# Performance work log

Measured on AMD Instinct MI355X. Metric: run time of the kernel, lower is better.

Reference implementation:

```python
import jax, jax.numpy as jnp
import numpy as np

N_HEAD = 16
N_KV = 4
N_EMBD = 2048
HEAD_DIM = N_EMBD // N_HEAD  # 128
GROUP = N_HEAD // N_KV       # 4 queries per kv head


def setup_inputs() -> dict:
    key = jax.random.key(0)
    ks = jax.random.split(key, 5)
    B, S = 2, 2048
    scale = 0.02
    return {
        "x": jax.random.normal(ks[0], (B, S, N_EMBD), dtype=jnp.float32),
        "Wq": jax.random.normal(ks[1], (N_EMBD, N_EMBD), dtype=jnp.float32) * scale,
        "Wk": jax.random.normal(ks[2], (N_EMBD, N_EMBD // GROUP), dtype=jnp.float32) * scale,
        "Wv": jax.random.normal(ks[3], (N_EMBD, N_EMBD // GROUP), dtype=jnp.float32) * scale,
        "Wo": jax.random.normal(ks[4], (N_EMBD, N_EMBD), dtype=jnp.float32) * scale,
    }


def reference(x, Wq, Wk, Wv, Wo):
    B, S, _ = x.shape
    scale = HEAD_DIM ** -0.5
    # projections (bias=False)
    q = (x @ Wq).reshape(B, S, N_KV, GROUP, HEAD_DIM)   # grouped query heads
    k = (x @ Wk).reshape(B, S, N_KV, HEAD_DIM)
    v = (x @ Wv).reshape(B, S, N_KV, HEAD_DIM)
    # scores: repeat_interleave of K over GROUP == broadcast over g axis
    scores = jnp.einsum('bqkgd,bskd->bkgqs', q, k) * scale  # [B,n_kv,g,S,S]
    causal = jnp.triu(jnp.ones((S, S), dtype=bool), k=1)
    scores = jnp.where(causal, jnp.finfo(scores.dtype).min, scores)
    attn = jax.nn.softmax(scores, axis=-1)
    out = jnp.einsum('bkgqs,bskd->bqkgd', attn, v)  # [B,S,n_kv,g,hd]
    out = out.reshape(B, S, N_EMBD)
    return out @ Wo
```

## Files before the change

kernel.cpp:

```cpp
#include <hip/hip_runtime.h>

typedef unsigned short u16;
typedef unsigned int u32;
typedef __attribute__((ext_vector_type(8))) __bf16 bh8;
typedef __attribute__((ext_vector_type(4))) float fx4;

#define AS1 __attribute__((address_space(1)))
#define AS3 __attribute__((address_space(3)))

__device__ __forceinline__ void gll16(const void* g, void* l) {
  void* gg = const_cast<void*>(g);
  __builtin_amdgcn_global_load_lds((AS1 void*)gg, (AS3 void*)l, 16, 0, 0);
}

__device__ __forceinline__ u16 f2b(float f) {
  union { float f; u32 u; } v; v.f = f;
  u32 r = v.u + 0x7FFFu + ((v.u >> 16) & 1u);
  return (u16)(r >> 16);
}

__device__ __forceinline__ fx4 fzero() { fx4 z = {0.f, 0.f, 0.f, 0.f}; return z; }

#define MFMA16(a, b, c) __builtin_amdgcn_mfma_f32_16x16x32_bf16(a, b, c, 0, 0, 0)

__global__ void k_cast(const float* __restrict__ in, u16* __restrict__ out, int n4) {
  int i = blockIdx.x * blockDim.x + threadIdx.x;
  if (i >= n4) return;
  float4 v = reinterpret_cast<const float4*>(in)[i];
  ushort4 o;
  o.x = f2b(v.x); o.y = f2b(v.y); o.z = f2b(v.z); o.w = f2b(v.w);
  reinterpret_cast<ushort4*>(out)[i] = o;
}

__global__ void k_transpose_cast(const float* __restrict__ in, u16* __restrict__ out,
                                 int R, int C) {
  __shared__ float t[32][33];
  int tx = threadIdx.x, ty = threadIdx.y;
  int r0 = blockIdx.y * 32, c0 = blockIdx.x * 32;
#pragma unroll
  for (int j = 0; j < 4; j++)
    t[ty + 8 * j][tx] = in[(size_t)(r0 + ty + 8 * j) * C + c0 + tx];
  __syncthreads();
#pragma unroll
  for (int j = 0; j < 4; j++)
    out[(size_t)(c0 + ty + 8 * j) * R + r0 + tx] = f2b(t[tx][ty + 8 * j]);
}

__global__ void k_transpose_v(const u16* __restrict__ in, u16* __restrict__ out) {
  __shared__ u16 t[32][33];
  int tx = threadIdx.x, ty = threadIdx.y;
  int s0 = blockIdx.x * 32, d0 = blockIdx.y * 32;
  int z = blockIdx.z, b = z >> 2, kv = z & 3;
#pragma unroll
  for (int j = 0; j < 4; j++)
    t[ty + 8 * j][tx] = in[(size_t)(b * 2048 + s0 + ty + 8 * j) * 512 + kv * 128 + d0 + tx];
  __syncthreads();
#pragma unroll
  for (int j = 0; j < 4; j++)
    out[(size_t)(z * 128 + d0 + ty + 8 * j) * 2048 + s0 + tx] = t[tx][ty + 8 * j];
}

__device__ __forceinline__ void gemm_core(const u16* __restrict__ A, const u16* __restrict__ Bt,
                                          int bm, int bn, u16* As, u16* Bs, fx4 acc[4][4]) {
  const int tid = threadIdx.x;
  const int lane = tid & 63, w = tid >> 6;
  const int wr = w >> 1, wc = w & 1;
  const int i = lane & 15, g = lane >> 4;
  const int c0 = tid, c1 = tid + 256;
  const u16* ga0 = A + (size_t)(bm + (c0 >> 2)) * 2048 + (c0 & 3) * 8;
  const u16* ga1 = A + (size_t)(bm + (c1 >> 2)) * 2048 + (c1 & 3) * 8;
  const u16* gb0 = Bt + (size_t)(bn + (c0 >> 2)) * 2048 + (c0 & 3) * 8;
  const u16* gb1 = Bt + (size_t)(bn + (c1 >> 2)) * 2048 + (c1 & 3) * 8;
  u16* la0 = As + c0 * 8; u16* la1 = As + c1 * 8;
  u16* lb0 = Bs + c0 * 8; u16* lb1 = Bs + c1 * 8;
  const u16* ra = As + (wr * 64 + i) * 32 + g * 8;
  const u16* rb = Bs + (wc * 64 + i) * 32 + g * 8;
  for (int kt = 0; kt < 2048; kt += 32) {
    __syncthreads();
    gll16(ga0 + kt, la0);
    gll16(ga1 + kt, la1);
    gll16(gb0 + kt, lb0);
    gll16(gb1 + kt, lb1);
    __syncthreads();
    bh8 af[4], bfr[4];
#pragma unroll
    for (int m = 0; m < 4; m++) af[m] = *reinterpret_cast<const bh8*>(ra + m * 16 * 32);
#pragma unroll
    for (int n = 0; n < 4; n++) bfr[n] = *reinterpret_cast<const bh8*>(rb + n * 16 * 32);
#pragma unroll
    for (int m = 0; m < 4; m++)
#pragma unroll
      for (int n = 0; n < 4; n++)
        acc[m][n] = MFMA16(af[m], bfr[n], acc[m][n]);
  }
}

__global__ __launch_bounds__(256, 3) void k_proj(const u16* __restrict__ xb,
                                                 const u16* __restrict__ Wqt,
                                                 const u16* __restrict__ Wkt,
                                                 const u16* __restrict__ Wvt,
                                                 u16* __restrict__ Qb, u16* __restrict__ Kb,
                                                 u16* __restrict__ Vb) {
  __shared__ __align__(16) u16 As[128 * 32];
  __shared__ __align__(16) u16 Bs[128 * 32];
  int by = blockIdx.y;
  const u16* Bt; u16* Cp; int bn, ldc; float alpha;
  if (by < 16)      { Bt = Wqt; Cp = Qb; bn = by * 128;        ldc = 2048; alpha = 0.08838834764831845f; }
  else if (by < 20) { Bt = Wkt; Cp = Kb; bn = (by - 16) * 128; ldc = 512;  alpha = 1.0f; }
  else              { Bt = Wvt; Cp = Vb; bn = (by - 20) * 128; ldc = 512;  alpha = 1.0f; }
  int bm = blockIdx.x * 128;
  fx4 acc[4][4];
#pragma unroll
  for (int m = 0; m < 4; m++)
#pragma unroll
    for (int n = 0; n < 4; n++) acc[m][n] = fzero();
  gemm_core(xb, Bt, bm, bn, As, Bs, acc);
  const int lane = threadIdx.x & 63, w = threadIdx.x >> 6;
  const int wr = w >> 1, wc = w & 1, i = lane & 15, g = lane >> 4;
#pragma unroll
  for (int m = 0; m < 4; m++)
#pragma unroll
    for (int n = 0; n < 4; n++)
#pragma unroll
      for (int r = 0; r < 4; r++) {
        int row = bm + wr * 64 + m * 16 + 4 * g + r;
        int col = bn + wc * 64 + n * 16 + i;
        Cp[(size_t)row * ldc + col] = f2b(acc[m][n][r] * alpha);
      }
}

__global__ __launch_bounds__(256, 3) void k_gemm_out(const u16* __restrict__ Ob,
                                                     const u16* __restrict__ Wot,
                                                     float* __restrict__ C) {
  __shared__ __align__(16) u16 As[128 * 32];
  __shared__ __align__(16) u16 Bs[128 * 32];
  int bm = blockIdx.x * 128, bn = blockIdx.y * 128;
  fx4 acc[4][4];
#pragma unroll
  for (int m = 0; m < 4; m++)
#pragma unroll
    for (int n = 0; n < 4; n++) acc[m][n] = fzero();
  gemm_core(Ob, Wot, bm, bn, As, Bs, acc);
  const int lane = threadIdx.x & 63, w = threadIdx.x >> 6;
  const int wr = w >> 1, wc = w & 1, i = lane & 15, g = lane >> 4;
#pragma unroll
  for (int m = 0; m < 4; m++)
#pragma unroll
    for (int n = 0; n < 4; n++)
#pragma unroll
      for (int r = 0; r < 4; r++) {
        int row = bm + wr * 64 + m * 16 + 4 * g + r;
        int col = bn + wc * 64 + n * 16 + i;
        C[(size_t)row * 2048 + col] = acc[m][n][r];
      }
}

__global__ __launch_bounds__(512, 4) void k_attn(const u16* __restrict__ Qb,
                                                 const u16* __restrict__ Kb,
                                                 const u16* __restrict__ Vt,
                                                 u16* __restrict__ Ob) {
  __shared__ __align__(16) u16 Ks0[64 * 128], Ks1[64 * 128];
  __shared__ __align__(16) u16 Vs0[128 * 64], Vs1[128 * 64];
  __shared__ __align__(16) u16 Pl[8][16 * 64];
  const int tid = threadIdx.x, lane = tid & 63, w = tid >> 6;
  const int i = lane & 15, g = lane >> 4;
  const int j = blockIdx.x;
  const int head = blockIdx.y, b = blockIdx.z, kv = head >> 2;
  const bool isA = (w >= 4);
  const int qt = isA ? j : (31 - j);
  const int qmin = qt * 64 + (w & 3) * 16;
  const int nt = 32 - j;
  const int myNt = isA ? (j + 1) : nt;

  const u16* Kbb = Kb + (size_t)b * 2048 * 512 + kv * 128;
  const u16* Vbb = Vt + (size_t)(b * 4 + kv) * 128 * 2048;

  bh8 qf[4];
  {
    const u16* qp = Qb + (size_t)(b * 2048 + qmin + i) * 2048 + head * 128 + g * 8;
#pragma unroll
    for (int kb = 0; kb < 4; kb++) qf[kb] = *reinterpret_cast<const bh8*>(qp + kb * 32);
  }

  fx4 o[8];
#pragma unroll
  for (int dt = 0; dt < 8; dt++) o[dt] = fzero();
  float m[4] = {-1e30f, -1e30f, -1e30f, -1e30f};
  float lp[4] = {0.f, 0.f, 0.f, 0.f};

  auto STAGE = [&](u16* Kd, u16* Vd, int s0) {
#pragma unroll
    for (int cc = 0; cc < 2; cc++) {
      int c = tid + cc * 512;
      gll16(Kbb + (size_t)(s0 + (c >> 4)) * 512 + (((c & 15) ^ ((c >> 4) & 7)) * 8),
            Kd + c * 8);
      gll16(Vbb + (size_t)(c >> 3) * 2048 + s0 + (((c & 7) ^ ((c >> 3) & 7)) * 8),
            Vd + c * 8);
    }
  };

  auto TILE = [&](const u16* Kbuf, const u16* Vbuf, int s0) {
    fx4 sc[4];
    __builtin_amdgcn_s_setprio(1);
#pragma unroll
    for (int st = 0; st < 4; st++) {
      sc[st] = fzero();
#pragma unroll
      for (int kb = 0; kb < 4; kb++) {
        bh8 kf = *reinterpret_cast<const bh8*>(Kbuf + (st * 16 + i) * 128 +
                                               (((kb * 4 + g) ^ (i & 7)) * 8));
        sc[st] = MFMA16(qf[kb], kf, sc[st]);
      }
    }
    __builtin_amdgcn_s_setprio(0);
    if (s0 + 63 > qmin) {
#pragma unroll
      for (int st = 0; st < 4; st++)
#pragma unroll
        for (int r = 0; r < 4; r++) {
          int s = s0 + st * 16 + i;
          int q = qmin + 4 * g + r;
          if (s > q) sc[st][r] = -1e30f;
        }
    }
    float pmax[4];
#pragma unroll
    for (int r = 0; r < 4; r++) {
      float v = fmaxf(fmaxf(sc[0][r], sc[1][r]), fmaxf(sc[2][r], sc[3][r]));
      v = fmaxf(v, __shfl_xor(v, 1));
      v = fmaxf(v, __shfl_xor(v, 2));
      v = fmaxf(v, __shfl_xor(v, 4));
      v = fmaxf(v, __shfl_xor(v, 8));
      pmax[r] = v;
    }
    int need = 0;
#pragma unroll
    for (int r = 0; r < 4; r++) need |= (pmax[r] > m[r] + 8.0f) ? 1 : 0;
    if (__any(need)) {
#pragma unroll
      for (int r = 0; r < 4; r++) {
        float mn = fmaxf(m[r], pmax[r]);
        float corr = __expf(m[r] - mn);
        m[r] = mn;
        lp[r] *= corr;
#pragma unroll
        for (int dt = 0; dt < 8; dt++) o[dt][r] *= corr;
      }
    }
    float p[4][4];
#pragma unroll
    for (int r = 0; r < 4; r++) {
#pragma unroll
      for (int st = 0; st < 4; st++) p[st][r] = __expf(sc[st][r] - m[r]);
      lp[r] += (p[0][r] + p[1][r]) + (p[2][r] + p[3][r]);
    }

#pragma unroll
    for (int st = 0; st < 4; st++)
#pragma unroll
      for (int r = 0; r < 4; r++) {
        int row = 4 * g + r;
        int cg = st * 2 + (i >> 3);
        Pl[w][row * 64 + ((cg ^ (row & 7)) << 3) + (i & 7)] = f2b(p[st][r]);
      }
    bh8 pf0 = *reinterpret_cast<const bh8*>(&Pl[w][i * 64 + ((g ^ (i & 7)) << 3)]);
    bh8 pf1 = *reinterpret_cast<const bh8*>(&Pl[w][i * 64 + (((4 + g) ^ (i & 7)) << 3)]);
    __builtin_amdgcn_s_setprio(1);
#pragma unroll
    for (int dt = 0; dt < 8; dt++) {
      bh8 v0 = *reinterpret_cast<const bh8*>(Vbuf + (dt * 16 + i) * 64 +
                                             ((g ^ (i & 7)) * 8));
      bh8 v1 = *reinterpret_cast<const bh8*>(Vbuf + (dt * 16 + i) * 64 +
                                             (((4 + g) ^ (i & 7)) * 8));
      o[dt] = MFMA16(pf0, v0, o[dt]);
      o[dt] = MFMA16(pf1, v1, o[dt]);
    }
    __builtin_amdgcn_s_setprio(0);
  };

  STAGE(Ks0, Vs0, 0);
  __syncthreads();
  for (int t = 0; t < nt; t += 2) {
    if (t + 1 < nt) STAGE(Ks1, Vs1, (t + 1) * 64);
    if (t < myNt) TILE(Ks0, Vs0, t * 64);
    __syncthreads();
    if (t + 1 >= nt) break;
    if (t + 2 < nt) STAGE(Ks0, Vs0, (t + 2) * 64);
    if (t + 1 < myNt) TILE(Ks1, Vs1, (t + 1) * 64);
    __syncthreads();
  }

#pragma unroll
  for (int r = 0; r < 4; r++) {
    float s = lp[r];
    s += __shfl_xor(s, 1);
    s += __shfl_xor(s, 2);
    s += __shfl_xor(s, 4);
    s += __shfl_xor(s, 8);
    float inv = 1.0f / s;
#pragma unroll
    for (int dt = 0; dt < 8; dt++)
      Ob[(size_t)(b * 2048 + qmin + 4 * g + r) * 2048 + head * 128 + dt * 16 + i] =
          f2b(o[dt][r] * inv);
  }
}

extern "C" void kernel_launch(void* const* d_in, const int* in_sizes, int n_in,
                              void* d_out, int out_size, void* d_ws, size_t ws_size,
                              hipStream_t stream) {
  (void)in_sizes; (void)n_in; (void)out_size; (void)ws_size;
  const float* x  = (const float*)d_in[0];
  const float* Wq = (const float*)d_in[1];
  const float* Wk = (const float*)d_in[2];
  const float* Wv = (const float*)d_in[3];
  const float* Wo = (const float*)d_in[4];

  char* ws = (char*)d_ws;
  size_t off = 0;
  auto alloc = [&](size_t bytes) {
    void* p = ws + off;
    off += (bytes + 255) & ~(size_t)255;
    return p;
  };
  u16* xb  = (u16*)alloc(8388608ull * 2);
  u16* Wqt = (u16*)alloc(4194304ull * 2);
  u16* Wkt = (u16*)alloc(1048576ull * 2);
  u16* Wvt = (u16*)alloc(1048576ull * 2);
  u16* Wot = (u16*)alloc(4194304ull * 2);
  u16* Qb  = (u16*)alloc(8388608ull * 2);
  u16* Kb  = (u16*)alloc(2097152ull * 2);
  u16* Vb  = (u16*)alloc(2097152ull * 2);
  u16* Vt  = (u16*)alloc(2097152ull * 2);
  u16* Ob  = xb;

  k_cast<<<8192, 256, 0, stream>>>(x, xb, 2097152);
  k_transpose_cast<<<dim3(64, 64), dim3(32, 8), 0, stream>>>(Wq, Wqt, 2048, 2048);
  k_transpose_cast<<<dim3(16, 64), dim3(32, 8), 0, stream>>>(Wk, Wkt, 2048, 512);
  k_transpose_cast<<<dim3(16, 64), dim3(32, 8), 0, stream>>>(Wv, Wvt, 2048, 512);
  k_transpose_cast<<<dim3(64, 64), dim3(32, 8), 0, stream>>>(Wo, Wot, 2048, 2048);
  k_proj<<<dim3(32, 24), 256, 0, stream>>>(xb, Wqt, Wkt, Wvt, Qb, Kb, Vb);
  k_transpose_v<<<dim3(64, 4, 8), dim3(32, 8), 0, stream>>>(Vb, Vt);
  k_attn<<<dim3(16, 16, 2), 512, 0, stream>>>(Qb, Kb, Vt, Ob);
  k_gemm_out<<<dim3(32, 16), 256, 0, stream>>>(Ob, Wot, (float*)d_out);
}
```

Baseline: 330.0 us.

## Use 256x256 double-buffered swizzled GEMM tiles for projection and output GEMMs

Replaces the 128x128, BK=32, single-buffered GEMM core with a 256x256 tile computed by 512 threads. It uses BK=64, XOR-swizzled LDS, and double buffering, so the next tile's global-to-LDS loads are issued between MFMA groups, with s_setprio raised around the MFMAs. The Q/K/V projections now index one concatenated transposed weight through a single pointer, which relies on Wkt and Wvt sitting right after Wqt in memory. The aim is more data reuse per LDS load and hidden load latency. The cost is far fewer blocks: 192 for the projection and 128 for the output GEMM, which may leave many CUs idle.

```diff
diff --git a/kernel.cpp b/kernel.cpp
--- a/kernel.cpp
+++ b/kernel.cpp
@@ -60,98 +60,126 @@
     out[(size_t)(z * 128 + d0 + ty + 8 * j) * 2048 + s0 + tx] = t[tx][ty + 8 * j];
 }
 
-__device__ __forceinline__ void gemm_core(const u16* __restrict__ A, const u16* __restrict__ Bt,
-                                          int bm, int bn, u16* As, u16* Bs, fx4 acc[4][4]) {
+__device__ __forceinline__ void gemm256(const u16* __restrict__ A, const u16* __restrict__ Bt,
+                                        int bm, int bn, u16* Sm, fx4 (&acc)[8][4]) {
+  u16* As = Sm;
+  u16* Bs = Sm + 32768;
   const int tid = threadIdx.x;
-  const int lane = tid & 63, w = tid >> 6;
-  const int wr = w >> 1, wc = w & 1;
+  const int lane = tid & 63;
   const int i = lane & 15, g = lane >> 4;
-  const int c0 = tid, c1 = tid + 256;
-  const u16* ga0 = A + (size_t)(bm + (c0 >> 2)) * 2048 + (c0 & 3) * 8;
-  const u16* ga1 = A + (size_t)(bm + (c1 >> 2)) * 2048 + (c1 & 3) * 8;
-  const u16* gb0 = Bt + (size_t)(bn + (c0 >> 2)) * 2048 + (c0 & 3) * 8;
-  const u16* gb1 = Bt + (size_t)(bn + (c1 >> 2)) * 2048 + (c1 & 3) * 8;
-  u16* la0 = As + c0 * 8; u16* la1 = As + c1 * 8;
-  u16* lb0 = Bs + c0 * 8; u16* lb1 = Bs + c1 * 8;
-  const u16* ra = As + (wr * 64 + i) * 32 + g * 8;
-  const u16* rb = Bs + (wc * 64 + i) * 32 + g * 8;
-  for (int kt = 0; kt < 2048; kt += 32) {
+  const int w = tid >> 6;
+  const int wr = w >> 2, wc = w & 3;
+  const int arow0 = wr * 128 + i;
+  const int brow0 = wc * 64 + i;
+  const int swz = i & 7;
+
+  auto SHALF = [&](const u16* G, int grow0, u16* Ld, int kt) {
+#pragma unroll
+    for (int cc = 0; cc < 2; cc++) {
+      int p = tid + cc * 512;
+      int row = p >> 3;
+      int lg = (p & 7) ^ (row & 7);
+      gll16(G + (size_t)(grow0 + row) * 2048 + kt + lg * 8, Ld + p * 8);
+    }
+  };
+
+  auto ITER = [&](const u16* cA, const u16* cB, u16* nA, u16* nB, int ktn, bool st) {
+    bh8 bf[4][2];
+#pragma unroll
+    for (int nf = 0; nf < 4; nf++)
+#pragma unroll
+      for (int kk = 0; kk < 2; kk++)
+        bf[nf][kk] = *reinterpret_cast<const bh8*>(
+            cB + (brow0 + nf * 16) * 64 + (((kk * 4 + g) ^ swz) << 3));
+#pragma unroll
+    for (int mp = 0; mp < 4; mp++) {
+      if (st && mp == 0) { SHALF(A, bm, nA, ktn); SHALF(Bt, bn, nB, ktn); }
+      if (st && mp == 1) { SHALF(A, bm + 128, nA + 8192, ktn); SHALF(Bt, bn + 128, nB + 8192, ktn); }
+      bh8 af[2][2];
+#pragma unroll
+      for (int mm = 0; mm < 2; mm++)
+#pragma unroll
+        for (int kk = 0; kk < 2; kk++)
+          af[mm][kk] = *reinterpret_cast<const bh8*>(
+              cA + (arow0 + (mp * 2 + mm) * 16) * 64 + (((kk * 4 + g) ^ swz) << 3));
+      __builtin_amdgcn_s_setprio(1);
+#pragma unroll
+      for (int mm = 0; mm < 2; mm++)
+#pragma unroll
+        for (int nf = 0; nf < 4; nf++)
+#pragma unroll
+          for (int kk = 0; kk < 2; kk++)
+            acc[mp * 2 + mm][nf] = MFMA16(af[mm][kk], bf[nf][kk], acc[mp * 2 + mm][nf]);
+      __builtin_amdgcn_s_setprio(0);
+    }
+  };
+
+  SHALF(A, bm, As, 0); SHALF(A, bm + 128, As + 8192, 0);
+  SHALF(Bt, bn, Bs, 0); SHALF(Bt, bn + 128, Bs + 8192, 0);
+  __syncthreads();
+  for (int t = 0; t < 32; t += 2) {
+    ITER(As, Bs, As + 16384, Bs + 16384, (t + 1) * 64, true);
     __syncthreads();
-    gll16(ga0 + kt, la0);
-    gll16(ga1 + kt, la1);
-    gll16(gb0 + kt, lb0);
-    gll16(gb1 + kt, lb1);
+    ITER(As + 16384, Bs + 16384, As, Bs, (t + 2) * 64, t + 2 < 32);
     __syncthreads();
-    bh8 af[4], bfr[4];
-#pragma unroll
-    for (int m = 0; m < 4; m++) af[m] = *reinterpret_cast<const bh8*>(ra + m * 16 * 32);
-#pragma unroll
-    for (int n = 0; n < 4; n++) bfr[n] = *reinterpret_cast<const bh8*>(rb + n * 16 * 32);
-#pragma unroll
-    for (int m = 0; m < 4; m++)
-#pragma unroll
-      for (int n = 0; n < 4; n++)
-        acc[m][n] = MFMA16(af[m], bfr[n], acc[m][n]);
   }
 }
 
-__global__ __launch_bounds__(256, 3) void k_proj(const u16* __restrict__ xb,
-                                                 const u16* __restrict__ Wqt,
-                                                 const u16* __restrict__ Wkt,
-                                                 const u16* __restrict__ Wvt,
+__global__ __launch_bounds__(512, 2) void k_proj(const u16* __restrict__ xb,
+                                                 const u16* __restrict__ Wt,
                                                  u16* __restrict__ Qb, u16* __restrict__ Kb,
                                                  u16* __restrict__ Vb) {
-  __shared__ __align__(16) u16 As[128 * 32];
-  __shared__ __align__(16) u16 Bs[128 * 32];
-  int by = blockIdx.y;
-  const u16* Bt; u16* Cp; int bn, ldc; float alpha;
-  if (by < 16)      { Bt = Wqt; Cp = Qb; bn = by * 128;        ldc = 2048; alpha = 0.08838834764831845f; }
-  else if (by < 20) { Bt = Wkt; Cp = Kb; bn = (by - 16) * 128; ldc = 512;  alpha = 1.0f; }
-  else              { Bt = Wvt; Cp = Vb; bn = (by - 20) * 128; ldc = 512;  alpha = 1.0f; }
-  int bm = blockIdx.x * 128;
-  fx4 acc[4][4];
-#pragma unroll
-  for (int m = 0; m < 4; m++)
+  __shared__ __align__(16) u16 Sm[65536];
+  fx4 acc[8][4];
+#pragma unroll
+  for (int m = 0; m < 8; m++)
 #pragma unroll
     for (int n = 0; n < 4; n++) acc[m][n] = fzero();
-  gemm_core(xb, Bt, bm, bn, As, Bs, acc);
+  const int bm = blockIdx.x * 256, by = blockIdx.y, bn = by * 256;
+  gemm256(xb, Wt, bm, bn, Sm, acc);
+
+  u16* Cp; int coff, ldc; float alpha;
+  if (by < 8)       { Cp = Qb; coff = by * 256;        ldc = 2048; alpha = 0.08838834764831845f; }
+  else if (by < 10) { Cp = Kb; coff = (by - 8) * 256;  ldc = 512;  alpha = 1.0f; }
+  else              { Cp = Vb; coff = (by - 10) * 256; ldc = 512;  alpha = 1.0f; }
+
   const int lane = threadIdx.x & 63, w = threadIdx.x >> 6;
-  const int wr = w >> 1, wc = w & 1, i = lane & 15, g = lane >> 4;
-#pragma unroll
-  for (int m = 0; m < 4; m++)
-#pragma unroll
-    for (int n = 0; n < 4; n++)
+  const int wr = w >> 2, wc = w & 3, i = lane & 15, g = lane >> 4;
+#pragma unroll
+  for (int mf = 0; mf < 8; mf++)
+#pragma unroll
+    for (int nf = 0; nf < 4; nf++)
 #pragma unroll
       for (int r = 0; r < 4; r++) {
-        int row = bm + wr * 64 + m * 16 + 4 * g + r;
-        int col = bn + wc * 64 + n * 16 + i;
-        Cp[(size_t)row * ldc + col] = f2b(acc[m][n][r] * alpha);
-      }
-}
-
-__global__ __launch_bounds__(256, 3) void k_gemm_out(const u16* __restrict__ Ob,
+        int row = bm + wr * 128 + mf * 16 + 4 * g + r;
+        int col = coff + wc * 64 + nf * 16 + i;
+        Cp[(size_t)row * ldc + col] = f2b(acc[mf][nf][r] * alpha);
+      }
+}
+
+__global__ __launch_bounds__(512, 2) void k_gemm_out(const u16* __restrict__ Ob,
                                                      const u16* __restrict__ Wot,
                                                      float* __restrict__ C) {
-  __shared__ __align__(16) u16 As[128 * 32];
-  __shared__ __align__(16) u16 Bs[128 * 32];
-  int bm = blockIdx.x * 128, bn = blockIdx.y * 128;
-  fx4 acc[4][4];
-#pragma unroll
-  for (int m = 0; m < 4; m++)
+  __shared__ __align__(16) u16 Sm[65536];
+  fx4 acc[8][4];
+#pragma unroll
+  for (int m = 0; m < 8; m++)
 #pragma unroll
     for (int n = 0; n < 4; n++) acc[m][n] = fzero();
-  gemm_core(Ob, Wot, bm, bn, As, Bs, acc);
+  const int bm = blockIdx.x * 256, bn = blockIdx.y * 256;
+  gemm256(Ob, Wot, bm, bn, Sm, acc);
+
   const int lane = threadIdx.x & 63, w = threadIdx.x >> 6;
-  const int wr = w >> 1, wc = w & 1, i = lane & 15, g = lane >> 4;
-#pragma unroll
-  for (int m = 0; m < 4; m++)
-#pragma unroll
-    for (int n = 0; n < 4; n++)
+  const int wr = w >> 2, wc = w & 3, i = lane & 15, g = lane >> 4;
+#pragma unroll
+  for (int mf = 0; mf < 8; mf++)
+#pragma unroll
+    for (int nf = 0; nf < 4; nf++)
 #pragma unroll
       for (int r = 0; r < 4; r++) {
-        int row = bm + wr * 64 + m * 16 + 4 * g + r;
-        int col = bn + wc * 64 + n * 16 + i;
-        C[(size_t)row * 2048 + col] = acc[m][n][r];
+        int row = bm + wr * 128 + mf * 16 + 4 * g + r;
+        int col = bn + wc * 64 + nf * 16 + i;
+        C[(size_t)row * 2048 + col] = acc[mf][nf][r];
       }
 }
 
@@ -338,8 +366,8 @@
   k_transpose_cast<<<dim3(16, 64), dim3(32, 8), 0, stream>>>(Wk, Wkt, 2048, 512);
   k_transpose_cast<<<dim3(16, 64), dim3(32, 8), 0, stream>>>(Wv, Wvt, 2048, 512);
   k_transpose_cast<<<dim3(64, 64), dim3(32, 8), 0, stream>>>(Wo, Wot, 2048, 2048);
-  k_proj<<<dim3(32, 24), 256, 0, stream>>>(xb, Wqt, Wkt, Wvt, Qb, Kb, Vb);
+  k_proj<<<dim3(16, 12), 512, 0, stream>>>(xb, Wqt, Qb, Kb, Vb);
   k_transpose_v<<<dim3(64, 4, 8), dim3(32, 8), 0, stream>>>(Vb, Vt);
   k_attn<<<dim3(16, 16, 2), 512, 0, stream>>>(Qb, Kb, Vt, Ob);
-  k_gemm_out<<<dim3(32, 16), 256, 0, stream>>>(Ob, Wot, (float*)d_out);
-}
+  k_gemm_out<<<dim3(16, 8), 512, 0, stream>>>(Ob, Wot, (float*)d_out);
+}
```

After: 323.0 us. -2.1%, faster.
